# Kernel tuning notes

Measured on AMD Instinct MI355X. Metric: run time of the kernel, lower is better.

The kernel has to match this reference:

```python
import jax, jax.numpy as jnp
import numpy as np

B, T, N, C, H = 64, 12, 1370, 8, 64

def setup_inputs() -> dict:
    key = jax.random.key(0)
    ks = jax.random.split(key, 7)
    s_ih = 1.0 / np.sqrt(H)
    inp = {
        "x": jax.random.normal(ks[0], (B, T, N, C), dtype=jnp.float32),
        # PyTorch nn.LSTM params, gate order (i, f, g, o)
        "W_ih": jax.random.uniform(ks[1], (4 * H, C), jnp.float32, -s_ih, s_ih),
        "W_hh": jax.random.uniform(ks[2], (4 * H, H), jnp.float32, -s_ih, s_ih),
        "b_ih": jax.random.uniform(ks[3], (4 * H,), jnp.float32, -s_ih, s_ih),
        "b_hh": jax.random.uniform(ks[4], (4 * H,), jnp.float32, -s_ih, s_ih),
        "W_fc": jax.random.uniform(ks[5], (C, H), jnp.float32, -s_ih, s_ih),
        "b_fc": jax.random.uniform(ks[6], (C,), jnp.float32, -s_ih, s_ih),
    }
    return inp

def reference(x, W_ih, W_hh, b_ih, b_hh, W_fc, b_fc):
    Bx, Tx, Nx, Cx = x.shape
    Hh = W_hh.shape[1]
    # (B, T, N, C) -> (B*N, T, C): shared-weight LSTM over all node sequences
    xr = jnp.transpose(x, (0, 2, 1, 3)).reshape(Bx * Nx, Tx, Cx)
    # Precompute input projections for all timesteps: (B*N, T, 4H)
    x_gates = jnp.einsum('btc,gc->btg', xr, W_ih) + b_ih
    # time-major for scan: (T, B*N, 4H)
    x_gates = jnp.moveaxis(x_gates, 1, 0)

    def step(carry, xg):
        h, c = carry
        gates = xg + h @ W_hh.T + b_hh  # (B*N, 4H)
        i, f, g, o = jnp.split(gates, 4, axis=-1)
        i = jax.nn.sigmoid(i)
        f = jax.nn.sigmoid(f)
        g = jnp.tanh(g)
        o = jax.nn.sigmoid(o)
        c = f * c + i * g
        h = o * jnp.tanh(c)
        return (h, c), None

    h0 = jnp.zeros((Bx * Nx, Hh), dtype=x.dtype)
    c0 = jnp.zeros((Bx * Nx, Hh), dtype=x.dtype)
    (h_last, _), _ = jax.lax.scan(step, (h0, c0), x_gates)

    y_flat = h_last @ W_fc.T + b_fc  # (B*N, C)
    return y_flat.reshape(Bx, Nx, Cx)
```

## Files before the change

### kernel.cpp

```cpp
#include <hip/hip_runtime.h>

#define T_ 12
#define N_ 1370
#define MSEQ 32
#define LDA 72
#define LDX 20
#define NBLK 2740

typedef __attribute__((ext_vector_type(8))) short short8;
typedef __attribute__((ext_vector_type(4))) float floatx4;

#define NLOG2E -1.4426950408889634f
#define TLOG2E 2.8853900817779268f

__device__ __forceinline__ short f2bf(float x) {
  unsigned u = __builtin_bit_cast(unsigned, x);
  u = (u + 0x7fffu + ((u >> 16) & 1u)) >> 16;
  return (short)u;
}
__device__ __forceinline__ unsigned pk_bf16(float a, float b) {
  unsigned r;
  asm("v_cvt_pk_bf16_f32 %0, %1, %2" : "=v"(r) : "v"(a), "v"(b));
  return r;
}
__device__ __forceinline__ short8 load_w8s(const float* __restrict__ p, float s) {
  short8 r;
#pragma unroll
  for (int j = 0; j < 8; ++j) r[j] = f2bf(p[j] * s);
  return r;
}

__global__ void __launch_bounds__(256, 4) lstm_kernel(
    const float* __restrict__ x, const float* __restrict__ W_ih,
    const float* __restrict__ W_hh, const float* __restrict__ b_ih,
    const float* __restrict__ b_hh, const float* __restrict__ W_fc,
    const float* __restrict__ b_fc, float* __restrict__ out) {
  __shared__ short hbuf[2][MSEQ][LDA];
  __shared__ short xls[T_][MSEQ][LDX];

  const int tid = threadIdx.x;
  const int wave = tid >> 6;
  const int lane = tid & 63;
  const int m16 = lane & 15;
  const int q = lane >> 4;
  const int blk = blockIdx.x;

  const int urow = wave * 16 + m16;
  short8 wA[4][3];
#pragma unroll
  for (int g = 0; g < 4; ++g) {
    const float sg = (g == 2) ? TLOG2E : NLOG2E;
    const int grow = g * 64 + urow;
    const float* wr = W_hh + grow * 64;
    wA[g][0] = load_w8s(wr + q * 8, sg);
    wA[g][1] = load_w8s(wr + 32 + q * 8, sg);
    short8 z = {0, 0, 0, 0, 0, 0, 0, 0};
    if (q == 0) {
      wA[g][2] = load_w8s(W_ih + grow * 8, sg);
    } else if (q == 1) {
      z[0] = f2bf(sg * (b_ih[grow] + b_hh[grow]));
      wA[g][2] = z;
    } else {
      wA[g][2] = z;
    }
  }

  {
    int* hp = (int*)hbuf;
#pragma unroll
    for (int i = tid; i < (2 * MSEQ * LDA) / 2; i += 256) hp[i] = 0;
    int* xp = (int*)xls;
#pragma unroll
    for (int i = tid; i < (T_ * MSEQ * LDX) / 2; i += 256) xp[i] = 0;
  }
  __syncthreads();

  {
    const int xseq = tid >> 3, xc = tid & 7;
    const int s0 = blk * MSEQ + xseq;
    const int bidx = s0 / N_;
    const int nidx = s0 - bidx * N_;
    const float* xp = x + ((size_t)(bidx * T_) * N_ + nidx) * 8 + xc;
#pragma unroll
    for (int t = 0; t < T_; ++t) {
      xls[t][xseq][xc] = f2bf(xp[(size_t)t * (N_ * 8)]);
      if (xc == 0) xls[t][xseq][8] = (short)0x3F80;
    }
  }
  __syncthreads();

  const int xoff = q ? 8 : 0;
  const floatx4 zacc = {0.0f, 0.0f, 0.0f, 0.0f};

  float cst[2][4];
#pragma unroll
  for (int nt = 0; nt < 2; ++nt)
#pragma unroll
    for (int r = 0; r < 4; ++r) cst[nt][r] = 0.0f;

  for (int t = 0; t < T_; ++t) {
    const int rb = t & 1, wb = rb ^ 1;
#pragma unroll
    for (int nt = 0; nt < 2; ++nt) {
      const int srow = nt * 16 + m16;
      short8 b0 = *(const short8*)&hbuf[rb][srow][q * 8];
      short8 b1 = *(const short8*)&hbuf[rb][srow][32 + q * 8];
      short8 bx = *(const short8*)&xls[t][srow][xoff];
      floatx4 gi = __builtin_amdgcn_mfma_f32_16x16x32_bf16(wA[0][0], b0, zacc, 0, 0, 0);
      floatx4 gf = __builtin_amdgcn_mfma_f32_16x16x32_bf16(wA[1][0], b0, zacc, 0, 0, 0);
      floatx4 gg = __builtin_amdgcn_mfma_f32_16x16x32_bf16(wA[2][0], b0, zacc, 0, 0, 0);
      floatx4 go = __builtin_amdgcn_mfma_f32_16x16x32_bf16(wA[3][0], b0, zacc, 0, 0, 0);
      gi = __builtin_amdgcn_mfma_f32_16x16x32_bf16(wA[0][1], b1, gi, 0, 0, 0);
      gf = __builtin_amdgcn_mfma_f32_16x16x32_bf16(wA[1][1], b1, gf, 0, 0, 0);
      gg = __builtin_amdgcn_mfma_f32_16x16x32_bf16(wA[2][1], b1, gg, 0, 0, 0);
      go = __builtin_amdgcn_mfma_f32_16x16x32_bf16(wA[3][1], b1, go, 0, 0, 0);
      gi = __builtin_amdgcn_mfma_f32_16x16x32_bf16(wA[0][2], bx, gi, 0, 0, 0);
      gf = __builtin_amdgcn_mfma_f32_16x16x32_bf16(wA[1][2], bx, gf, 0, 0, 0);
      gg = __builtin_amdgcn_mfma_f32_16x16x32_bf16(wA[2][2], bx, gg, 0, 0, 0);
      go = __builtin_amdgcn_mfma_f32_16x16x32_bf16(wA[3][2], bx, go, 0, 0, 0);
      float hv[4];
#pragma unroll
      for (int r = 0; r < 4; ++r) {
        float di = 1.0f + __builtin_amdgcn_exp2f(gi[r]);
        float df = 1.0f + __builtin_amdgcn_exp2f(gf[r]);
        float dg = 1.0f + __builtin_amdgcn_exp2f(gg[r]);
        float dq = 1.0f + __builtin_amdgcn_exp2f(go[r]);
        float pa = di * df, pb = dg * dq;
        float rp = __builtin_amdgcn_rcpf(pa * pb);
        float iv = rp * df * pb;
        float fv = rp * di * pb;
        float gv = fmaf(-2.0f, rp * pa * dq, 1.0f);
        float ov = rp * pa * dg;
        float cc = fmaf(fv, cst[nt][r], iv * gv);
        cst[nt][r] = cc;
        float dt = 1.0f + __builtin_amdgcn_exp2f(cc * TLOG2E);
        float tc = fmaf(-2.0f, __builtin_amdgcn_rcpf(dt), 1.0f);
        hv[r] = ov * tc;
      }
      unsigned long long pk =
          (unsigned long long)pk_bf16(hv[0], hv[1]) |
          ((unsigned long long)pk_bf16(hv[2], hv[3]) << 32);
      *(unsigned long long*)&hbuf[wb][srow][wave * 16 + q * 4] = pk;
    }
    __syncthreads();
  }

  if (wave < 2) {
    short8 f0, f1;
    short8 z = {0, 0, 0, 0, 0, 0, 0, 0};
    if (m16 < 8) {
      const float* wr = W_fc + m16 * 64;
      f0 = load_w8s(wr + q * 8, 1.0f);
      f1 = load_w8s(wr + 32 + q * 8, 1.0f);
    } else {
      f0 = z;
      f1 = z;
    }
    const int srow = wave * 16 + m16;
    short8 h0 = *(const short8*)&hbuf[0][srow][q * 8];
    short8 h1 = *(const short8*)&hbuf[0][srow][32 + q * 8];
    floatx4 acc = __builtin_amdgcn_mfma_f32_16x16x32_bf16(f0, h0, zacc, 0, 0, 0);
    acc = __builtin_amdgcn_mfma_f32_16x16x32_bf16(f1, h1, acc, 0, 0, 0);
    if (q < 2) {
      const int orow = blk * MSEQ + srow;
#pragma unroll
      for (int r = 0; r < 4; ++r)
        out[orow * 8 + q * 4 + r] = acc[r] + b_fc[q * 4 + r];
    }
  }
}

extern "C" void kernel_launch(void* const* d_in, const int* in_sizes, int n_in,
                              void* d_out, int out_size, void* d_ws,
                              size_t ws_size, hipStream_t stream) {
  const float* x    = (const float*)d_in[0];
  const float* W_ih = (const float*)d_in[1];
  const float* W_hh = (const float*)d_in[2];
  const float* b_ih = (const float*)d_in[3];
  const float* b_hh = (const float*)d_in[4];
  const float* W_fc = (const float*)d_in[5];
  const float* b_fc = (const float*)d_in[6];
  float* out = (float*)d_out;
  hipLaunchKernelGGL(lstm_kernel, dim3(NBLK), dim3(256), 0, stream,
                     x, W_ih, W_hh, b_ih, b_hh, W_fc, b_fc, out);
}
```

Baseline: 170.1 us.

## Double sequences per block, compact x staging, prescale cell state

Each block now processes 64 sequences instead of 32, running four 16-row tiles per wave, so weights are loaded once for twice as many sequences and half as many blocks are launched. The x staging buffer is packed to 8 bf16 values per row, filled with vectorized float4 loads, and the bias column comes from a shared ones row. The cell state is kept pre-scaled by 2·log2(e), which removes a multiply before the tanh exp2. Weight loads use float4 reads and packed bf16 conversion. The costs are more register pressure per thread and fewer blocks to spread over the CUs.

```diff
diff --git a/kernel.cpp b/kernel.cpp
--- a/kernel.cpp
+++ b/kernel.cpp
@@ -2,16 +2,19 @@
 
 #define T_ 12
 #define N_ 1370
-#define MSEQ 32
+#define MSEQ 64
+#define NT 4
 #define LDA 72
-#define LDX 20
-#define NBLK 2740
+#define NBLK 1370
 
 typedef __attribute__((ext_vector_type(8))) short short8;
 typedef __attribute__((ext_vector_type(4))) float floatx4;
+typedef __attribute__((ext_vector_type(4))) unsigned uint4v;
+typedef __attribute__((ext_vector_type(2))) unsigned uint2v;
 
 #define NLOG2E -1.4426950408889634f
 #define TLOG2E 2.8853900817779268f
+#define N2LOG2E -5.7707801635558536f
 
 __device__ __forceinline__ short f2bf(float x) {
   unsigned u = __builtin_bit_cast(unsigned, x);
@@ -24,10 +27,11 @@
   return r;
 }
 __device__ __forceinline__ short8 load_w8s(const float* __restrict__ p, float s) {
-  short8 r;
-#pragma unroll
-  for (int j = 0; j < 8; ++j) r[j] = f2bf(p[j] * s);
-  return r;
+  floatx4 a = *(const floatx4*)p;
+  floatx4 b = *(const floatx4*)(p + 4);
+  uint4v u = {pk_bf16(a[0] * s, a[1] * s), pk_bf16(a[2] * s, a[3] * s),
+              pk_bf16(b[0] * s, b[1] * s), pk_bf16(b[2] * s, b[3] * s)};
+  return __builtin_bit_cast(short8, u);
 }
 
 __global__ void __launch_bounds__(256, 4) lstm_kernel(
@@ -36,7 +40,8 @@
     const float* __restrict__ b_hh, const float* __restrict__ W_fc,
     const float* __restrict__ b_fc, float* __restrict__ out) {
   __shared__ short hbuf[2][MSEQ][LDA];
-  __shared__ short xls[T_][MSEQ][LDX];
+  __shared__ __align__(16) short xbuf[T_][MSEQ][8];
+  __shared__ __align__(16) short ones_row[8];
 
   const int tid = threadIdx.x;
   const int wave = tid >> 6;
@@ -69,43 +74,45 @@
     int* hp = (int*)hbuf;
 #pragma unroll
     for (int i = tid; i < (2 * MSEQ * LDA) / 2; i += 256) hp[i] = 0;
-    int* xp = (int*)xls;
-#pragma unroll
-    for (int i = tid; i < (T_ * MSEQ * LDX) / 2; i += 256) xp[i] = 0;
+    if (tid < 8) ones_row[tid] = (tid == 0) ? (short)0x3F80 : (short)0;
   }
-  __syncthreads();
 
   {
-    const int xseq = tid >> 3, xc = tid & 7;
-    const int s0 = blk * MSEQ + xseq;
-    const int bidx = s0 / N_;
-    const int nidx = s0 - bidx * N_;
-    const float* xp = x + ((size_t)(bidx * T_) * N_ + nidx) * 8 + xc;
 #pragma unroll
-    for (int t = 0; t < T_; ++t) {
-      xls[t][xseq][xc] = f2bf(xp[(size_t)t * (N_ * 8)]);
-      if (xc == 0) xls[t][xseq][8] = (short)0x3F80;
+    for (int j = 0; j < 6; ++j) {
+      const int slot = j * 256 + tid;
+      const int t = slot >> 7;
+      const int idx = slot & 127;
+      const int seq = idx >> 1;
+      const int half = idx & 1;
+      const int s0 = blk * MSEQ + seq;
+      const int bidx = s0 / N_;
+      const int nidx = s0 - bidx * N_;
+      const floatx4 v = *(const floatx4*)(
+          x + (((size_t)bidx * T_ + t) * N_ + nidx) * 8 + half * 4);
+      uint2v u = {pk_bf16(v[0], v[1]), pk_bf16(v[2], v[3])};
+      *(uint2v*)&xbuf[t][seq][half * 4] = u;
     }
   }
   __syncthreads();
 
-  const int xoff = q ? 8 : 0;
   const floatx4 zacc = {0.0f, 0.0f, 0.0f, 0.0f};
 
-  float cst[2][4];
+  float cst[NT][4];
 #pragma unroll
-  for (int nt = 0; nt < 2; ++nt)
+  for (int nt = 0; nt < NT; ++nt)
 #pragma unroll
     for (int r = 0; r < 4; ++r) cst[nt][r] = 0.0f;
 
   for (int t = 0; t < T_; ++t) {
     const int rb = t & 1, wb = rb ^ 1;
 #pragma unroll
-    for (int nt = 0; nt < 2; ++nt) {
+    for (int nt = 0; nt < NT; ++nt) {
       const int srow = nt * 16 + m16;
       short8 b0 = *(const short8*)&hbuf[rb][srow][q * 8];
       short8 b1 = *(const short8*)&hbuf[rb][srow][32 + q * 8];
-      short8 bx = *(const short8*)&xls[t][srow][xoff];
+      const short* bxp = q ? &ones_row[0] : &xbuf[t][srow][0];
+      short8 bx = *(const short8*)bxp;
       floatx4 gi = __builtin_amdgcn_mfma_f32_16x16x32_bf16(wA[0][0], b0, zacc, 0, 0, 0);
       floatx4 gf = __builtin_amdgcn_mfma_f32_16x16x32_bf16(wA[1][0], b0, zacc, 0, 0, 0);
       floatx4 gg = __builtin_amdgcn_mfma_f32_16x16x32_bf16(wA[2][0], b0, zacc, 0, 0, 0);
@@ -127,13 +134,14 @@
         float dq = 1.0f + __builtin_amdgcn_exp2f(go[r]);
         float pa = di * df, pb = dg * dq;
         float rp = __builtin_amdgcn_rcpf(pa * pb);
-        float iv = rp * df * pb;
         float fv = rp * di * pb;
-        float gv = fmaf(-2.0f, rp * pa * dq, 1.0f);
-        float ov = rp * pa * dg;
-        float cc = fmaf(fv, cst[nt][r], iv * gv);
-        cst[nt][r] = cc;
-        float dt = 1.0f + __builtin_amdgcn_exp2f(cc * TLOG2E);
+        float rpa = rp * pa;
+        float ov = rpa * dg;
+        float tg = fmaf(TLOG2E, dg, N2LOG2E);
+        float ig = tg * rp * (df * dq);
+        float cs = fmaf(fv, cst[nt][r], ig);
+        cst[nt][r] = cs;
+        float dt = 1.0f + __builtin_amdgcn_exp2f(cs);
         float tc = fmaf(-2.0f, __builtin_amdgcn_rcpf(dt), 1.0f);
         hv[r] = ov * tc;
       }
@@ -145,7 +153,7 @@
     __syncthreads();
   }
 
-  if (wave < 2) {
+  {
     short8 f0, f1;
     short8 z = {0, 0, 0, 0, 0, 0, 0, 0};
     if (m16 < 8) {
```

New measurement: 170.6 us. Within noise of the previous version (+0.3%).

## Batch both sequence tiles' MFMAs before activations and fold c scaling into state

Applied to the files above, without the earlier changes.

Restructures the timestep loop so all LDS loads for both 16-sequence tiles come first, then all 24 MFMAs, then all exp2 evaluations, then the cell update. This exposes more independent work to hide MFMA and transcendental latency. The cell state is now kept pre-scaled by 2*log2(e), which removes one multiply per element. The launch bound drops from 4 to 3 waves per SIMD so the extra live registers fit, which may lower occupancy.

```diff
diff --git a/kernel.cpp b/kernel.cpp
--- a/kernel.cpp
+++ b/kernel.cpp
@@ -12,6 +12,7 @@
 
 #define NLOG2E -1.4426950408889634f
 #define TLOG2E 2.8853900817779268f
+#define N2LOG2E -5.7707801635558536f
 
 __device__ __forceinline__ short f2bf(float x) {
   unsigned u = __builtin_bit_cast(unsigned, x);
@@ -30,7 +31,7 @@
   return r;
 }
 
-__global__ void __launch_bounds__(256, 4) lstm_kernel(
+__global__ void __launch_bounds__(256, 3) lstm_kernel(
     const float* __restrict__ x, const float* __restrict__ W_ih,
     const float* __restrict__ W_hh, const float* __restrict__ b_ih,
     const float* __restrict__ b_hh, const float* __restrict__ W_fc,
@@ -100,47 +101,63 @@
 
   for (int t = 0; t < T_; ++t) {
     const int rb = t & 1, wb = rb ^ 1;
+
+    short8 b0[2], b1[2], bx[2];
 #pragma unroll
     for (int nt = 0; nt < 2; ++nt) {
       const int srow = nt * 16 + m16;
-      short8 b0 = *(const short8*)&hbuf[rb][srow][q * 8];
-      short8 b1 = *(const short8*)&hbuf[rb][srow][32 + q * 8];
-      short8 bx = *(const short8*)&xls[t][srow][xoff];
-      floatx4 gi = __builtin_amdgcn_mfma_f32_16x16x32_bf16(wA[0][0], b0, zacc, 0, 0, 0);
-      floatx4 gf = __builtin_amdgcn_mfma_f32_16x16x32_bf16(wA[1][0], b0, zacc, 0, 0, 0);
-      floatx4 gg = __builtin_amdgcn_mfma_f32_16x16x32_bf16(wA[2][0], b0, zacc, 0, 0, 0);
-      floatx4 go = __builtin_amdgcn_mfma_f32_16x16x32_bf16(wA[3][0], b0, zacc, 0, 0, 0);
-      gi = __builtin_amdgcn_mfma_f32_16x16x32_bf16(wA[0][1], b1, gi, 0, 0, 0);
-      gf = __builtin_amdgcn_mfma_f32_16x16x32_bf16(wA[1][1], b1, gf, 0, 0, 0);
-      gg = __builtin_amdgcn_mfma_f32_16x16x32_bf16(wA[2][1], b1, gg, 0, 0, 0);
-      go = __builtin_amdgcn_mfma_f32_16x16x32_bf16(wA[3][1], b1, go, 0, 0, 0);
-      gi = __builtin_amdgcn_mfma_f32_16x16x32_bf16(wA[0][2], bx, gi, 0, 0, 0);
-      gf = __builtin_amdgcn_mfma_f32_16x16x32_bf16(wA[1][2], bx, gf, 0, 0, 0);
-      gg = __builtin_amdgcn_mfma_f32_16x16x32_bf16(wA[2][2], bx, gg, 0, 0, 0);
-      go = __builtin_amdgcn_mfma_f32_16x16x32_bf16(wA[3][2], bx, go, 0, 0, 0);
+      b0[nt] = *(const short8*)&hbuf[rb][srow][q * 8];
+      b1[nt] = *(const short8*)&hbuf[rb][srow][32 + q * 8];
+      bx[nt] = *(const short8*)&xls[t][srow][xoff];
+    }
+
+    floatx4 acc[2][4];
+#pragma unroll
+    for (int nt = 0; nt < 2; ++nt)
+#pragma unroll
+      for (int g = 0; g < 4; ++g) {
+        floatx4 c = __builtin_amdgcn_mfma_f32_16x16x32_bf16(wA[g][0], b0[nt], zacc, 0, 0, 0);
+        c = __builtin_amdgcn_mfma_f32_16x16x32_bf16(wA[g][1], b1[nt], c, 0, 0, 0);
+        c = __builtin_amdgcn_mfma_f32_16x16x32_bf16(wA[g][2], bx[nt], c, 0, 0, 0);
+        acc[nt][g] = c;
+      }
+
+    float di[2][4], df[2][4], dg_[2][4], dq_[2][4];
+#pragma unroll
+    for (int nt = 0; nt < 2; ++nt)
+#pragma unroll
+      for (int r = 0; r < 4; ++r) {
+        di[nt][r] = 1.0f + __builtin_amdgcn_exp2f(acc[nt][0][r]);
+        df[nt][r] = 1.0f + __builtin_amdgcn_exp2f(acc[nt][1][r]);
+        dg_[nt][r] = 1.0f + __builtin_amdgcn_exp2f(acc[nt][2][r]);
+        dq_[nt][r] = 1.0f + __builtin_amdgcn_exp2f(acc[nt][3][r]);
+      }
+    unsigned long long pkv[2];
+#pragma unroll
+    for (int nt = 0; nt < 2; ++nt) {
       float hv[4];
 #pragma unroll
       for (int r = 0; r < 4; ++r) {
-        float di = 1.0f + __builtin_amdgcn_exp2f(gi[r]);
-        float df = 1.0f + __builtin_amdgcn_exp2f(gf[r]);
-        float dg = 1.0f + __builtin_amdgcn_exp2f(gg[r]);
-        float dq = 1.0f + __builtin_amdgcn_exp2f(go[r]);
-        float pa = di * df, pb = dg * dq;
+        float pa = di[nt][r] * df[nt][r], pb = dg_[nt][r] * dq_[nt][r];
         float rp = __builtin_amdgcn_rcpf(pa * pb);
-        float iv = rp * df * pb;
-        float fv = rp * di * pb;
-        float gv = fmaf(-2.0f, rp * pa * dq, 1.0f);
-        float ov = rp * pa * dg;
-        float cc = fmaf(fv, cst[nt][r], iv * gv);
-        cst[nt][r] = cc;
-        float dt = 1.0f + __builtin_amdgcn_exp2f(cc * TLOG2E);
+        float fv = rp * di[nt][r] * pb;
+        float ov = rp * pa * dg_[nt][r];
+        float tg = fmaf(TLOG2E, dg_[nt][r], N2LOG2E);
+        float ig = tg * rp * (df[nt][r] * dq_[nt][r]);
+        float cs = fmaf(fv, cst[nt][r], ig);
+        cst[nt][r] = cs;
+        float dt = 1.0f + __builtin_amdgcn_exp2f(cs);
         float tc = fmaf(-2.0f, __builtin_amdgcn_rcpf(dt), 1.0f);
         hv[r] = ov * tc;
       }
-      unsigned long long pk =
-          (unsigned long long)pk_bf16(hv[0], hv[1]) |
-          ((unsigned long long)pk_bf16(hv[2], hv[3]) << 32);
-      *(unsigned long long*)&hbuf[wb][srow][wave * 16 + q * 4] = pk;
+      pkv[nt] = (unsigned long long)pk_bf16(hv[0], hv[1]) |
+                ((unsigned long long)pk_bf16(hv[2], hv[3]) << 32);
+    }
+
+#pragma unroll
+    for (int nt = 0; nt < 2; ++nt) {
+      const int srow = nt * 16 + m16;
+      *(unsigned long long*)&hbuf[wb][srow][wave * 16 + q * 4] = pkv[nt];
     }
     __syncthreads();
   }
```

After: 172.4 us. No clear change (+1.4%).
